# Kernel optimization log

Hardware: AMD Instinct MI355X
Metric: run time of the kernel (lower is better)

## Reference

```python
import jax, jax.numpy as jnp
import numpy as np

NUM_HEADS = 16

def setup_inputs() -> dict:
    key = jax.random.key(0)
    ks = jax.random.split(key, 11)
    B, S, D = 4, 1024, 1024
    M = 128
    hd = D // NUM_HEADS
    s = 0.02
    return {
        'x':  jax.random.normal(ks[0], (B, S, D), jnp.float32),
        'Wq': jax.random.normal(ks[1], (D, D), jnp.float32) * s,
        'bq': jax.random.normal(ks[2], (D,), jnp.float32) * s,
        'Wk': jax.random.normal(ks[3], (D, D), jnp.float32) * s,
        'bk': jax.random.normal(ks[4], (D,), jnp.float32) * s,
        'Wv': jax.random.normal(ks[5], (D, D), jnp.float32) * s,
        'bv': jax.random.normal(ks[6], (D,), jnp.float32) * s,
        'Wo': jax.random.normal(ks[7], (D, D), jnp.float32) * s,
        'bo': jax.random.normal(ks[8], (D,), jnp.float32) * s,
        'rel_k': jax.random.normal(ks[9], (2 * M + 1, hd), jnp.float32),
        'rel_v': jax.random.normal(ks[10], (2 * M + 1, hd), jnp.float32),
    }

def reference(x, Wq, bq, Wk, bk, Wv, bv, Wo, bo, rel_k, rel_v):
    B, S, D = x.shape
    H = NUM_HEADS
    hd = D // H
    M = (rel_k.shape[0] - 1) // 2

    def proj(W, b):
        # torch nn.Linear: x @ W.T + b, then split heads -> [B,H,S,hd]
        return (x @ W.T + b).reshape(B, S, H, hd).transpose(0, 2, 1, 3)

    q = proj(Wq, bq)
    k = proj(Wk, bk)
    v = proj(Wv, bv)

    # relative position index matrix [S,S]: clip(j - i, -M, M) + M
    r = jnp.arange(S)
    idx = jnp.clip(r[None, :] - r[:, None], -M, M) + M
    rpk = rel_k[idx]  # [S,S,hd] (equivalent to one-hot matmul lookup)
    rpv = rel_v[idx]  # [S,S,hd]

    content = jnp.einsum('bhqd,bhkd->bhqk', q, k)
    relative = jnp.einsum('bhqd,qkd->bhqk', q, rpk)
    scores = (content + relative) / jnp.sqrt(jnp.float32(hd))
    w = jax.nn.softmax(scores, axis=-1)  # [B,H,S,S]

    out = jnp.einsum('bhqk,bhkd->bhqd', w, v) + jnp.einsum('bhqk,qkd->bhqd', w, rpv)
    out = out.transpose(0, 2, 1, 3).reshape(B, S, D)
    return out @ Wo.T + bo
```

## Files before the change

### kernel.cpp

```cpp
#include <hip/hip_runtime.h>
#include <hip/hip_bf16.h>
#include <math.h>

#define SEQ 1024
#define NH 16
#define HD 64
#define DM 1024
#define MWIN 128
#define RR 257

typedef __attribute__((ext_vector_type(8))) short bf16x8;
typedef __attribute__((ext_vector_type(4))) float f32x4;

__device__ __forceinline__ unsigned short f2b_bits(float f) {
  return __builtin_bit_cast(unsigned short, __float2bfloat16(f));
}
__device__ __forceinline__ float b2f(unsigned short u) {
  return __uint_as_float(((unsigned int)u) << 16);
}
__device__ __forceinline__ void gl16(const void* g, void* l) {
  __builtin_amdgcn_global_load_lds(
      (const __attribute__((address_space(1))) unsigned int*)g,
      (__attribute__((address_space(3))) unsigned int*)l, 16, 0, 0);
}

__global__ __launch_bounds__(256) void f2b_kernel(const float* __restrict__ in,
                                                  unsigned short* __restrict__ out,
                                                  int n4) {
  int i = blockIdx.x * 256 + threadIdx.x;
  const int stride = gridDim.x * 256;
  for (; i < n4; i += stride) {
    float4 v = ((const float4*)in)[i];
    ushort4 o;
    o.x = f2b_bits(v.x); o.y = f2b_bits(v.y); o.z = f2b_bits(v.z); o.w = f2b_bits(v.w);
    ((ushort4*)out)[i] = o;
  }
}

__global__ __launch_bounds__(256) void w4_conv(const float* __restrict__ w0,
                                               const float* __restrict__ w1,
                                               const float* __restrict__ w2,
                                               const float* __restrict__ w3,
                                               unsigned short* __restrict__ out) {
  int idx = blockIdx.x * 256 + threadIdx.x;
  const int m = idx >> 18, local = idx & 262143;
  const float* src = m == 0 ? w0 : (m == 1 ? w1 : (m == 2 ? w2 : w3));
  float4 v = ((const float4*)src)[local];
  ushort4 o;
  o.x = f2b_bits(v.x); o.y = f2b_bits(v.y); o.z = f2b_bits(v.z); o.w = f2b_bits(v.w);
  ((ushort4*)out)[idx] = o;
}

__global__ __launch_bounds__(256) void relk_conv(const float* __restrict__ rk,
                                                 unsigned short* __restrict__ out) {
  int idx = blockIdx.x * 256 + threadIdx.x;
  int r = idx >> 6;
  int rs = r > 256 ? 256 : r;
  out[idx] = f2b_bits(rk[rs * HD + (idx & 63)]);
}

__global__ __launch_bounds__(256) void relv_t(const float* __restrict__ rv,
                                              unsigned short* __restrict__ out) {
  int idx = blockIdx.x * 256 + threadIdx.x;
  if (idx >= 64 * 288) return;
  int d = idx / 288, r = idx % 288;
  out[idx] = (r < RR) ? f2b_bits(rv[(size_t)r * HD + d]) : (unsigned short)0;
}

__global__ __launch_bounds__(256) void qkv_gemm(const unsigned short* __restrict__ A,
                                                const unsigned short* __restrict__ Bw,
                                                const float* __restrict__ bq,
                                                const float* __restrict__ bk,
                                                const float* __restrict__ bv,
                                                unsigned short* __restrict__ Qo,
                                                unsigned short* __restrict__ Ko,
                                                unsigned short* __restrict__ Vo) {
  __shared__ unsigned short As[128 * 32];
  __shared__ unsigned short Bs[128 * 32];
  const int t = threadIdx.x;
  const int lane = t & 63;
  const int wave = t >> 6;
  const int wr = wave >> 1, wc = wave & 1;
  const int lrow = lane & 15, lk = lane >> 4;
  const int m0 = blockIdx.x * 128, n0 = blockIdx.y * 128;

  const int mat = n0 >> 10;
  const float* bias = mat == 0 ? bq : (mat == 1 ? bk : bv);
  unsigned short* Co = mat == 0 ? Qo : (mat == 1 ? Ko : Vo);
  const float scale = mat == 0 ? 0.125f : 1.0f;

  const unsigned short* Ag = A + (size_t)m0 * DM;
  const unsigned short* Bg = Bw + (size_t)n0 * DM;
  const int r0 = t >> 2, r1 = (t + 256) >> 2;
  const int c0 = (t & 3) << 3;

  f32x4 acc[4][4] = {};

  for (int k0 = 0; k0 < DM; k0 += 32) {
    __syncthreads();
    gl16(Ag + (size_t)r0 * DM + k0 + c0, &As[t * 8]);
    gl16(Bg + (size_t)r0 * DM + k0 + c0, &Bs[t * 8]);
    gl16(Ag + (size_t)r1 * DM + k0 + c0, &As[(t + 256) * 8]);
    gl16(Bg + (size_t)r1 * DM + k0 + c0, &Bs[(t + 256) * 8]);
    __syncthreads();
    bf16x8 af[4], bfr[4];
#pragma unroll
    for (int i = 0; i < 4; ++i)
      af[i] = *(const bf16x8*)&As[(wr * 64 + i * 16 + lrow) * 32 + lk * 8];
#pragma unroll
    for (int j = 0; j < 4; ++j)
      bfr[j] = *(const bf16x8*)&Bs[(wc * 64 + j * 16 + lrow) * 32 + lk * 8];
#pragma unroll
    for (int i = 0; i < 4; ++i)
#pragma unroll
      for (int j = 0; j < 4; ++j)
        acc[i][j] = __builtin_amdgcn_mfma_f32_16x16x32_bf16(af[i], bfr[j], acc[i][j], 0, 0, 0);
  }

  float bvv[4];
#pragma unroll
  for (int j = 0; j < 4; ++j) bvv[j] = bias[(n0 & 1023) + wc * 64 + j * 16 + lrow];

#pragma unroll
  for (int i = 0; i < 4; ++i) {
#pragma unroll
    for (int j = 0; j < 4; ++j) {
      const int nl = (n0 & 1023) + wc * 64 + j * 16 + lrow;
      const int h = nl >> 6, d = nl & 63;
#pragma unroll
      for (int r = 0; r < 4; ++r) {
        const int m = m0 + wr * 64 + i * 16 + lk * 4 + r;
        const int b = m >> 10, s = m & 1023;
        float v = (acc[i][j][r] + bvv[j]) * scale;
        Co[((size_t)(b * NH + h) * SEQ + s) * HD + d] = f2b_bits(v);
      }
    }
  }
}

template<int MODE>
__global__ __launch_bounds__(256) void mfma_gemm(const unsigned short* __restrict__ A,
                                                 const unsigned short* __restrict__ B,
                                                 const float* __restrict__ bias,
                                                 float* __restrict__ Cf,
                                                 unsigned short* __restrict__ Cb,
                                                 int K) {
  __shared__ unsigned short As[128 * 32];
  __shared__ unsigned short Bs[128 * 32];
  const int t = threadIdx.x;
  const int lane = t & 63;
  const int wave = t >> 6;
  const int wr = wave >> 1, wc = wave & 1;
  const int lrow = lane & 15, lk = lane >> 4;
  const int m0 = blockIdx.x * 128, n0 = blockIdx.y * 128;

  const unsigned short* Ag = A + (size_t)m0 * K;
  const unsigned short* Bg = B + (size_t)n0 * K;
  const int r0 = t >> 2, r1 = (t + 256) >> 2;
  const int c0 = (t & 3) << 3;

  f32x4 acc[4][4] = {};

  for (int k0 = 0; k0 < K; k0 += 32) {
    __syncthreads();
    gl16(Ag + (size_t)r0 * K + k0 + c0, &As[t * 8]);
    gl16(Bg + (size_t)r0 * K + k0 + c0, &Bs[t * 8]);
    gl16(Ag + (size_t)r1 * K + k0 + c0, &As[(t + 256) * 8]);
    gl16(Bg + (size_t)r1 * K + k0 + c0, &Bs[(t + 256) * 8]);
    __syncthreads();
    bf16x8 af[4], bfr[4];
#pragma unroll
    for (int i = 0; i < 4; ++i)
      af[i] = *(const bf16x8*)&As[(wr * 64 + i * 16 + lrow) * 32 + lk * 8];
#pragma unroll
    for (int j = 0; j < 4; ++j)
      bfr[j] = *(const bf16x8*)&Bs[(wc * 64 + j * 16 + lrow) * 32 + lk * 8];
#pragma unroll
    for (int i = 0; i < 4; ++i)
#pragma unroll
      for (int j = 0; j < 4; ++j)
        acc[i][j] = __builtin_amdgcn_mfma_f32_16x16x32_bf16(af[i], bfr[j], acc[i][j], 0, 0, 0);
  }

  float bvv[4];
  if (MODE == 1) {
#pragma unroll
    for (int j = 0; j < 4; ++j) bvv[j] = bias[n0 + wc * 64 + j * 16 + lrow];
  }
#pragma unroll
  for (int i = 0; i < 4; ++i) {
#pragma unroll
    for (int j = 0; j < 4; ++j) {
      const int n = n0 + wc * 64 + j * 16 + lrow;
#pragma unroll
      for (int r = 0; r < 4; ++r) {
        const int m = m0 + wr * 64 + i * 16 + lk * 4 + r;
        float v = acc[i][j][r];
        if (MODE == 1) {
          Cf[(size_t)m * DM + n] = v + bvv[j];
        } else {
          if (n < RR) Cb[(size_t)m * RR + n] = f2b_bits(v);
        }
      }
    }
  }
}

#define FLASH_LDS_BYTES 80896

__global__ __launch_bounds__(256) void flash_mfma(
    const unsigned short* __restrict__ Qb,
    const unsigned short* __restrict__ Kb,
    const unsigned short* __restrict__ Vb,
    const unsigned short* __restrict__ qrb,
    const unsigned short* __restrict__ relvT,
    unsigned short* __restrict__ attnb) {
  extern __shared__ char smem[];
  unsigned short* Ks = (unsigned short*)smem;
  unsigned short (*VT)[144]    = (unsigned short(*)[144])(smem + 16384);
  unsigned short (*Ps)[16][72] = (unsigned short(*)[16][72])(smem + 34816);
  unsigned short (*wrs)[288]   = (unsigned short(*)[288])(smem + 44032);

  const int t = threadIdx.x;
  const int lane = t & 63;
  const int w = t >> 6;
  const int lq = lane & 15;
  const int g  = lane >> 4;
  const int bh = blockIdx.y;
  const int q0 = blockIdx.x * 64;
  const int qw0 = q0 + w * 16;

  const unsigned short* Qp = Qb + (size_t)bh * SEQ * HD;
  const unsigned short* Kp = Kb + (size_t)bh * SEQ * HD;
  const unsigned short* Vp = Vb + (size_t)bh * SEQ * HD;

  {
    unsigned int* wz = (unsigned int*)(smem + 44032);
    for (int i = t; i < 9216; i += 256) wz[i] = 0u;
  }

  bf16x8 aq[2];
  aq[0] = *(const bf16x8*)(Qp + (size_t)(qw0 + lq) * HD + g * 8);
  aq[1] = *(const bf16x8*)(Qp + (size_t)(qw0 + lq) * HD + 32 + g * 8);

  const size_t qrow0 = ((size_t)bh * SEQ + qw0 + g * 4) * RR;
  float bq0[4], bq256[4];
#pragma unroll
  for (int rr = 0; rr < 4; ++rr) {
    bq0[rr]   = b2f(qrb[qrow0 + (size_t)rr * RR]);
    bq256[rr] = b2f(qrb[qrow0 + (size_t)rr * RR + 256]);
  }

  float l[4] = {}, accL[4] = {}, accR[4] = {};
  f32x4 out1[4] = {};

  const int p = lane;
  const int dvv = w * 16;
  bf16x8 v00 = *(const bf16x8*)(Vp + (size_t)(2 * p) * HD + dvv);
  bf16x8 v01 = *(const bf16x8*)(Vp + (size_t)(2 * p) * HD + dvv + 8);
  bf16x8 v10 = *(const bf16x8*)(Vp + (size_t)(2 * p + 1) * HD + dvv);
  bf16x8 v11 = *(const bf16x8*)(Vp + (size_t)(2 * p + 1) * HD + dvv + 8);

  for (int kt = 0; kt < 8; ++kt) {
    const int k0 = kt * 128;
    __syncthreads();

#pragma unroll
    for (int u = 0; u < 4; ++u) {
      const int ch = t + u * 256;
      const int row = ch >> 3;
      const int src = (row << 3) | ((ch & 7) ^ (row & 7));
      gl16(Kp + (size_t)k0 * HD + src * 8, &Ks[ch * 8]);
    }
#pragma unroll
    for (int j = 0; j < 8; ++j) {
      *(unsigned int*)&VT[dvv + j][2 * p] =
          (unsigned short)v00[j] | ((unsigned int)(unsigned short)v10[j] << 16);
      *(unsigned int*)&VT[dvv + 8 + j][2 * p] =
          (unsigned short)v01[j] | ((unsigned int)(unsigned short)v11[j] << 16);
    }

    const int dh0 = k0 - qw0, dh1 = dh0 + 64;
    const int cls0 = dh0 <= -192 ? 0 : (dh0 >= 144 ? 1 : 2);
    const int cls1 = dh1 <= -192 ? 0 : (dh1 >= 144 ? 1 : 2);
    float bias0[4][4], bias1[4][4];
    if (cls0 == 2) {
      const int dbase = dh0 + lq - g * 4;
#pragma unroll
      for (int j = 0; j < 4; ++j)
#pragma unroll
        for (int rr = 0; rr < 4; ++rr) {
          int delta = dbase + j * 16 - rr;
          int r = delta < -MWIN ? 0 : (delta > MWIN ? 256 : delta + MWIN);
          bias0[j][rr] = b2f(qrb[qrow0 + (size_t)rr * RR + r]);
        }
    }
    if (cls1 == 2) {
      const int dbase = dh1 + lq - g * 4;
#pragma unroll
      for (int j = 0; j < 4; ++j)
#pragma unroll
        for (int rr = 0; rr < 4; ++rr) {
          int delta = dbase + j * 16 - rr;
          int r = delta < -MWIN ? 0 : (delta > MWIN ? 256 : delta + MWIN);
          bias1[j][rr] = b2f(qrb[qrow0 + (size_t)rr * RR + r]);
        }
    }
    __syncthreads();

    if (kt < 7) {
      const unsigned short* Vn = Vp + (size_t)(k0 + 128) * HD + dvv;
      v00 = *(const bf16x8*)(Vn + (size_t)(2 * p) * HD);
      v01 = *(const bf16x8*)(Vn + (size_t)(2 * p) * HD + 8);
      v10 = *(const bf16x8*)(Vn + (size_t)(2 * p + 1) * HD);
      v11 = *(const bf16x8*)(Vn + (size_t)(2 * p + 1) * HD + 8);
    }

#pragma unroll
    for (int h = 0; h < 2; ++h) {
      const int dh = h == 0 ? dh0 : dh1;
      const int cls = h == 0 ? cls0 : cls1;
      const float (*bias)[4] = h == 0 ? bias0 : bias1;

      f32x4 sc[4] = {};
#pragma unroll
      for (int j = 0; j < 4; ++j) {
        const int row = h * 64 + j * 16 + lq;
#pragma unroll
        for (int kk = 0; kk < 2; ++kk) {
          const int ch = (kk * 4 + g) ^ (lq & 7);
          bf16x8 bk = *(const bf16x8*)&Ks[row * 64 + ch * 8];
          sc[j] = __builtin_amdgcn_mfma_f32_16x16x32_bf16(aq[kk], bk, sc[j], 0, 0, 0);
        }
      }

      float wvf[4][4], ssum[4] = {};
      if (cls == 2) {
#pragma unroll
        for (int j = 0; j < 4; ++j)
#pragma unroll
          for (int rr = 0; rr < 4; ++rr) {
            float wv = __expf(sc[j][rr] + bias[j][rr]);
            wvf[j][rr] = wv; ssum[rr] += wv;
          }
        const int dbase = dh + lq - g * 4;
#pragma unroll
        for (int j = 0; j < 4; ++j)
#pragma unroll
          for (int rr = 0; rr < 4; ++rr) {
            const unsigned short ub = f2b_bits(wvf[j][rr]);
            Ps[w][g * 4 + rr][j * 16 + lq] = ub;
            const int delta = dbase + j * 16 - rr;
            if (delta <= -MWIN)      accL[rr] += wvf[j][rr];
            else if (delta >= MWIN)  accR[rr] += wvf[j][rr];
            else                     wrs[w * 16 + g * 4 + rr][delta + MWIN] = ub;
          }
      } else {
        const float* bb = cls == 0 ? bq0 : bq256;
#pragma unroll
        for (int j = 0; j < 4; ++j)
#pragma unroll
          for (int rr = 0; rr < 4; ++rr) {
            float wv = __expf(sc[j][rr] + bb[rr]);
            wvf[j][rr] = wv; ssum[rr] += wv;
            Ps[w][g * 4 + rr][j * 16 + lq] = f2b_bits(wv);
          }
#pragma unroll
        for (int rr = 0; rr < 4; ++rr) {
          if (cls == 0) accL[rr] += ssum[rr]; else accR[rr] += ssum[rr];
        }
      }

#pragma unroll
      for (int rr = 0; rr < 4; ++rr) {
        float s0 = ssum[rr];
#pragma unroll
        for (int o = 1; o < 16; o <<= 1) s0 += __shfl_xor(s0, o);
        l[rr] += s0;
      }

      bf16x8 pa[2];
      pa[0] = *(const bf16x8*)&Ps[w][lq][g * 8];
      pa[1] = *(const bf16x8*)&Ps[w][lq][32 + g * 8];
#pragma unroll
      for (int jd = 0; jd < 4; ++jd) {
        const int vrow = jd * 16 + lq;
#pragma unroll
        for (int kk = 0; kk < 2; ++kk) {
          bf16x8 vb = *(const bf16x8*)&VT[vrow][h * 64 + kk * 32 + g * 8];
          out1[jd] = __builtin_amdgcn_mfma_f32_16x16x32_bf16(pa[kk], vb, out1[jd], 0, 0, 0);
        }
      }
    }
  }

#pragma unroll
  for (int rr = 0; rr < 4; ++rr) {
    float sL = accL[rr], sR = accR[rr];
#pragma unroll
    for (int o = 1; o < 16; o <<= 1) { sL += __shfl_xor(sL, o); sR += __shfl_xor(sR, o); }
    if (lq == 0) {
      wrs[w * 16 + g * 4 + rr][0]   = f2b_bits(sL);
      wrs[w * 16 + g * 4 + rr][256] = f2b_bits(sR);
    }
  }
  __syncthreads();

  f32x4 out2[4] = {};
#pragma unroll
  for (int kk = 0; kk < 9; ++kk) {
    bf16x8 pa2 = *(const bf16x8*)&wrs[w * 16 + lq][kk * 32 + g * 8];
#pragma unroll
    for (int jd = 0; jd < 4; ++jd) {
      bf16x8 vb = *(const bf16x8*)(relvT + (size_t)(jd * 16 + lq) * 288 + kk * 32 + g * 8);
      out2[jd] = __builtin_amdgcn_mfma_f32_16x16x32_bf16(pa2, vb, out2[jd], 0, 0, 0);
    }
  }

  const int b = bh >> 4, h = bh & 15;
#pragma unroll
  for (int jd = 0; jd < 4; ++jd)
#pragma unroll
    for (int rr = 0; rr < 4; ++rr) {
      const int s = qw0 + g * 4 + rr;
      const int d = jd * 16 + lq;
      float vout = (out1[jd][rr] + out2[jd][rr]) / l[rr];
      attnb[(size_t)(b * SEQ + s) * DM + h * HD + d] = f2b_bits(vout);
    }
}

extern "C" void kernel_launch(void* const* d_in, const int* in_sizes, int n_in,
                              void* d_out, int out_size, void* d_ws, size_t ws_size,
                              hipStream_t stream) {
  const float* x     = (const float*)d_in[0];
  const float* Wq    = (const float*)d_in[1];
  const float* bq    = (const float*)d_in[2];
  const float* Wk    = (const float*)d_in[3];
  const float* bk    = (const float*)d_in[4];
  const float* Wv    = (const float*)d_in[5];
  const float* bv    = (const float*)d_in[6];
  const float* Wo    = (const float*)d_in[7];
  const float* bo    = (const float*)d_in[8];
  const float* rel_k = (const float*)d_in[9];
  const float* rel_v = (const float*)d_in[10];
  float* out = (float*)d_out;

  unsigned short* us    = (unsigned short*)d_ws;
  unsigned short* qrb   = us;
  unsigned short* xb    = us + 16842752;
  unsigned short* attnb = xb;
  unsigned short* Wqb   = xb + 4194304;
  unsigned short* Wob   = Wqb + 3145728;
  unsigned short* Qbf   = Wob + 1048576;
  unsigned short* Kbb   = Qbf + 4194304;
  unsigned short* Vbb   = Kbb + 4194304;
  unsigned short* relkb = Vbb + 4194304;
  unsigned short* relvtb= relkb + 24576;

  f2b_kernel<<<2048, 256, 0, stream>>>(x, xb, 1048576);
  w4_conv<<<4096, 256, 0, stream>>>(Wq, Wk, Wv, Wo, Wqb);
  relk_conv<<<96, 256, 0, stream>>>(rel_k, relkb);
  relv_t<<<72, 256, 0, stream>>>(rel_v, relvtb);

  qkv_gemm<<<dim3(32, 24), 256, 0, stream>>>(xb, Wqb, bq, bk, bv, Qbf, Kbb, Vbb);

  mfma_gemm<2><<<dim3(512, 3), 256, 0, stream>>>(Qbf, relkb, nullptr, nullptr, qrb, HD);

  (void)hipFuncSetAttribute(reinterpret_cast<const void*>(flash_mfma),
                            hipFuncAttributeMaxDynamicSharedMemorySize,
                            FLASH_LDS_BYTES);
  flash_mfma<<<dim3(16, 64), 256, FLASH_LDS_BYTES, stream>>>(Qbf, Kbb, Vbb, qrb, relvtb, attnb);

  mfma_gemm<1><<<dim3(32, 8), 256, 0, stream>>>(attnb, Wob, bo, out, nullptr, DM);
}
```

Measured before the change: 249.6 us.

## Double flash block query tile to 128 and fuse input conversion kernels

The attention kernel now runs 512 threads (8 waves) per block covering 128 queries, so each K and V tile staged into LDS is shared by twice as many query rows. Each wave now loads only 8 of the V columns into the transposed V buffer. The per-wave score and probability buffers grow, raising LDS to about 124 KB per block, which cuts the grid in half and may limit occupancy to one block per CU. Separately, the four bf16 conversion and prep kernels are merged into a single launch that branches on block index, removing three launches.

Measured after the change: 240.9 us. 1.04x faster.

```diff
diff --git a/kernel.cpp b/kernel.cpp
--- a/kernel.cpp
+++ b/kernel.cpp
@@ -24,47 +24,44 @@
       (__attribute__((address_space(3))) unsigned int*)l, 16, 0, 0);
 }
 
-__global__ __launch_bounds__(256) void f2b_kernel(const float* __restrict__ in,
-                                                  unsigned short* __restrict__ out,
-                                                  int n4) {
-  int i = blockIdx.x * 256 + threadIdx.x;
-  const int stride = gridDim.x * 256;
-  for (; i < n4; i += stride) {
-    float4 v = ((const float4*)in)[i];
+__global__ __launch_bounds__(256) void prep_conv(const float* __restrict__ x,
+                                                 const float* __restrict__ w0,
+                                                 const float* __restrict__ w1,
+                                                 const float* __restrict__ w2,
+                                                 const float* __restrict__ w3,
+                                                 const float* __restrict__ rk,
+                                                 const float* __restrict__ rv,
+                                                 unsigned short* __restrict__ xb,
+                                                 unsigned short* __restrict__ wb,
+                                                 unsigned short* __restrict__ relkb,
+                                                 unsigned short* __restrict__ relvtb) {
+  const int bid = blockIdx.x, t = threadIdx.x;
+  if (bid < 4096) {
+    int i = bid * 256 + t;
+    float4 v = ((const float4*)x)[i];
     ushort4 o;
     o.x = f2b_bits(v.x); o.y = f2b_bits(v.y); o.z = f2b_bits(v.z); o.w = f2b_bits(v.w);
-    ((ushort4*)out)[i] = o;
-  }
-}
-
-__global__ __launch_bounds__(256) void w4_conv(const float* __restrict__ w0,
-                                               const float* __restrict__ w1,
-                                               const float* __restrict__ w2,
-                                               const float* __restrict__ w3,
-                                               unsigned short* __restrict__ out) {
-  int idx = blockIdx.x * 256 + threadIdx.x;
-  const int m = idx >> 18, local = idx & 262143;
-  const float* src = m == 0 ? w0 : (m == 1 ? w1 : (m == 2 ? w2 : w3));
-  float4 v = ((const float4*)src)[local];
-  ushort4 o;
-  o.x = f2b_bits(v.x); o.y = f2b_bits(v.y); o.z = f2b_bits(v.z); o.w = f2b_bits(v.w);
-  ((ushort4*)out)[idx] = o;
-}
-
-__global__ __launch_bounds__(256) void relk_conv(const float* __restrict__ rk,
-                                                 unsigned short* __restrict__ out) {
-  int idx = blockIdx.x * 256 + threadIdx.x;
-  int r = idx >> 6;
-  int rs = r > 256 ? 256 : r;
-  out[idx] = f2b_bits(rk[rs * HD + (idx & 63)]);
-}
-
-__global__ __launch_bounds__(256) void relv_t(const float* __restrict__ rv,
-                                              unsigned short* __restrict__ out) {
-  int idx = blockIdx.x * 256 + threadIdx.x;
-  if (idx >= 64 * 288) return;
-  int d = idx / 288, r = idx % 288;
-  out[idx] = (r < RR) ? f2b_bits(rv[(size_t)r * HD + d]) : (unsigned short)0;
+    ((ushort4*)xb)[i] = o;
+  } else if (bid < 8192) {
+    int idx = (bid - 4096) * 256 + t;
+    const int m = idx >> 18, local = idx & 262143;
+    const float* src = m == 0 ? w0 : (m == 1 ? w1 : (m == 2 ? w2 : w3));
+    float4 v = ((const float4*)src)[local];
+    ushort4 o;
+    o.x = f2b_bits(v.x); o.y = f2b_bits(v.y); o.z = f2b_bits(v.z); o.w = f2b_bits(v.w);
+    ((ushort4*)wb)[idx] = o;
+  } else if (bid < 8288) {
+    int idx = (bid - 8192) * 256 + t;
+    int r = idx >> 6;
+    int rs = r > 256 ? 256 : r;
+    relkb[idx] = f2b_bits(rk[rs * HD + (idx & 63)]);
+  } else {
+    int idx = (bid - 8288) * 256 + t;
+    if (idx < 64 * 288) {
+      int d = idx / 288, r = idx % 288;
+      relvtb[idx] = (r < RR) ? f2b_bits(rv[(size_t)r * HD + d]) : (unsigned short)0;
+    }
+  }
 }
 
 __global__ __launch_bounds__(256) void qkv_gemm(const unsigned short* __restrict__ A,
@@ -206,9 +203,9 @@
   }
 }
 
-#define FLASH_LDS_BYTES 80896
-
-__global__ __launch_bounds__(256) void flash_mfma(
+#define FLASH_LDS_BYTES 126976
+
+__global__ __launch_bounds__(512) void flash_mfma(
     const unsigned short* __restrict__ Qb,
     const unsigned short* __restrict__ Kb,
     const unsigned short* __restrict__ Vb,
@@ -219,7 +216,7 @@
   unsigned short* Ks = (unsigned short*)smem;
   unsigned short (*VT)[144]    = (unsigned short(*)[144])(smem + 16384);
   unsigned short (*Ps)[16][72] = (unsigned short(*)[16][72])(smem + 34816);
-  unsigned short (*wrs)[288]   = (unsigned short(*)[288])(smem + 44032);
+  unsigned short (*wrs)[288]   = (unsigned short(*)[288])(smem + 53248);
 
   const int t = threadIdx.x;
   const int lane = t & 63;
@@ -227,7 +224,7 @@
   const int lq = lane & 15;
   const int g  = lane >> 4;
   const int bh = blockIdx.y;
-  const int q0 = blockIdx.x * 64;
+  const int q0 = blockIdx.x * 128;
   const int qw0 = q0 + w * 16;
 
   const unsigned short* Qp = Qb + (size_t)bh * SEQ * HD;
@@ -235,8 +232,8 @@
   const unsigned short* Vp = Vb + (size_t)bh * SEQ * HD;
 
   {
-    unsigned int* wz = (unsigned int*)(smem + 44032);
-    for (int i = t; i < 9216; i += 256) wz[i] = 0u;
+    unsigned int* wz = (unsigned int*)(smem + 53248);
+    for (int i = t; i < 18432; i += 512) wz[i] = 0u;
   }
 
   bf16x8 aq[2];
@@ -254,30 +251,26 @@
   float l[4] = {}, accL[4] = {}, accR[4] = {};
   f32x4 out1[4] = {};
 
-  const int p = lane;
-  const int dvv = w * 16;
-  bf16x8 v00 = *(const bf16x8*)(Vp + (size_t)(2 * p) * HD + dvv);
-  bf16x8 v01 = *(const bf16x8*)(Vp + (size_t)(2 * p) * HD + dvv + 8);
-  bf16x8 v10 = *(const bf16x8*)(Vp + (size_t)(2 * p + 1) * HD + dvv);
-  bf16x8 v11 = *(const bf16x8*)(Vp + (size_t)(2 * p + 1) * HD + dvv + 8);
+  const int sv = 2 * lane;
+  const int dvv = w * 8;
+  bf16x8 v00 = *(const bf16x8*)(Vp + (size_t)sv * HD + dvv);
+  bf16x8 v10 = *(const bf16x8*)(Vp + (size_t)(sv + 1) * HD + dvv);
 
   for (int kt = 0; kt < 8; ++kt) {
     const int k0 = kt * 128;
     __syncthreads();
 
 #pragma unroll
-    for (int u = 0; u < 4; ++u) {
-      const int ch = t + u * 256;
+    for (int u = 0; u < 2; ++u) {
+      const int ch = t + u * 512;
       const int row = ch >> 3;
       const int src = (row << 3) | ((ch & 7) ^ (row & 7));
       gl16(Kp + (size_t)k0 * HD + src * 8, &Ks[ch * 8]);
     }
 #pragma unroll
     for (int j = 0; j < 8; ++j) {
-      *(unsigned int*)&VT[dvv + j][2 * p] =
+      *(unsigned int*)&VT[dvv + j][sv] =
           (unsigned short)v00[j] | ((unsigned int)(unsigned short)v10[j] << 16);
-      *(unsigned int*)&VT[dvv + 8 + j][2 * p] =
-          (unsigned short)v01[j] | ((unsigned int)(unsigned short)v11[j] << 16);
     }
 
     const int dh0 = k0 - qw0, dh1 = dh0 + 64;
@@ -310,10 +303,8 @@
 
     if (kt < 7) {
       const unsigned short* Vn = Vp + (size_t)(k0 + 128) * HD + dvv;
-      v00 = *(const bf16x8*)(Vn + (size_t)(2 * p) * HD);
-      v01 = *(const bf16x8*)(Vn + (size_t)(2 * p) * HD + 8);
-      v10 = *(const bf16x8*)(Vn + (size_t)(2 * p + 1) * HD);
-      v11 = *(const bf16x8*)(Vn + (size_t)(2 * p + 1) * HD + 8);
+      v00 = *(const bf16x8*)(Vn + (size_t)sv * HD);
+      v10 = *(const bf16x8*)(Vn + (size_t)(sv + 1) * HD);
     }
 
 #pragma unroll
@@ -457,10 +448,8 @@
   unsigned short* relkb = Vbb + 4194304;
   unsigned short* relvtb= relkb + 24576;
 
-  f2b_kernel<<<2048, 256, 0, stream>>>(x, xb, 1048576);
-  w4_conv<<<4096, 256, 0, stream>>>(Wq, Wk, Wv, Wo, Wqb);
-  relk_conv<<<96, 256, 0, stream>>>(rel_k, relkb);
-  relv_t<<<72, 256, 0, stream>>>(rel_v, relvtb);
+  prep_conv<<<8360, 256, 0, stream>>>(x, Wq, Wk, Wv, Wo, rel_k, rel_v,
+                                      xb, Wqb, relkb, relvtb);
 
   qkv_gemm<<<dim3(32, 24), 256, 0, stream>>>(xb, Wqb, bq, bk, bv, Qbf, Kbb, Vbb);
 
@@ -469,7 +458,7 @@
   (void)hipFuncSetAttribute(reinterpret_cast<const void*>(flash_mfma),
                             hipFuncAttributeMaxDynamicSharedMemorySize,
                             FLASH_LDS_BYTES);
-  flash_mfma<<<dim3(16, 64), 256, FLASH_LDS_BYTES, stream>>>(Qbf, Kbb, Vbb, qrb, relvtb, attnb);
+  flash_mfma<<<dim3(8, 64), 512, FLASH_LDS_BYTES, stream>>>(Qbf, Kbb, Vbb, qrb, relvtb, attnb);
 
   mfma_gemm<1><<<dim3(32, 8), 256, 0, stream>>>(attnb, Wob, bo, out, nullptr, DM);
 }
```
